# Performance work log

Hardware: AMD Instinct MI355X
Metric: run time of the kernel (lower is better)

The kernel has to match this reference:

```python
import jax, jax.numpy as jnp
import numpy as np

B, D, C, H = 16384, 512, 4096, 1024

def setup_inputs() -> dict:
    key = jax.random.key(0)
    k1, k2, k3, k4 = jax.random.split(key, 4)
    x = jax.random.normal(k1, (B, D), dtype=jnp.float32)
    centers = jax.random.normal(k2, (C, D), dtype=jnp.float32)
    # nn.Linear(C, H): weight [H, C], bias [H]
    W1 = jax.random.normal(k3, (H, C), dtype=jnp.float32) * (1.0 / np.sqrt(C))
    b1 = jax.random.normal(k4, (H,), dtype=jnp.float32) * 0.01
    return {"x": x, "centers": centers, "W1": W1, "b1": b1, "sigma": 1}


def reference(x, centers, W1, b1, sigma):
    sigma = jnp.float32(sigma)
    # Pairwise Euclidean distances via dot-product expansion (fused, no [B,C,D] tensor)
    x2 = jnp.sum(x * x, axis=-1, keepdims=True)            # [B, 1]
    c2 = jnp.sum(centers * centers, axis=-1)               # [C]
    xc = x @ centers.T                                     # [B, C]
    d2 = jnp.maximum(x2 + c2[None, :] - 2.0 * xc, 0.0)
    dists = jnp.sqrt(d2)                                   # [B, C]
    # Note: original uses exp(-dists / (2*sigma)) with UNSQUARED distance
    phi = jnp.exp(-dists / (2.0 * sigma))
    out = jax.nn.sigmoid(phi @ W1.T + b1)                  # [B, H]
    return out
```

## Files before the change

kernel.cpp:

```cpp
#include <hip/hip_runtime.h>
#include <hip/hip_bf16.h>

#define B_ROWS 16384
#define D_DIM  512
#define C_DIM  4096
#define H_DIM  1024

typedef __attribute__((ext_vector_type(8))) short  bf16x8;
typedef __attribute__((ext_vector_type(8))) unsigned short u16x8;
typedef __attribute__((ext_vector_type(4))) float  f32x4;

#define GLB __attribute__((address_space(1)))
#define LDS __attribute__((address_space(3)))

__device__ __forceinline__ unsigned short f2bf(float f) {
    unsigned int u = __float_as_uint(f);
    unsigned int r = (u + 0x7FFFu + ((u >> 16) & 1u)) >> 16;
    return (unsigned short)r;
}

__device__ __forceinline__ void async16(const void* g, void* l) {
    __builtin_amdgcn_global_load_lds((const GLB unsigned int*)g,
                                     (LDS unsigned int*)l, 16, 0, 0);
}

__device__ __forceinline__ float read_sigma(const int* p) {
    int v = *p;
    if (v >= 1 && v < (1 << 20)) return (float)v;
    return __int_as_float(v);
}

__global__ __launch_bounds__(64) void prep_rows(const float* __restrict__ in,
                                                unsigned short* __restrict__ outb,
                                                float* __restrict__ out2) {
    int row  = blockIdx.x;
    int lane = threadIdx.x;
    const float4* p = (const float4*)(in + (size_t)row * D_DIM) + lane * 2;
    float4 a = p[0], b = p[1];
    float s = a.x*a.x + a.y*a.y + a.z*a.z + a.w*a.w
            + b.x*b.x + b.y*b.y + b.z*b.z + b.w*b.w;
    u16x8 o = { f2bf(a.x), f2bf(a.y), f2bf(a.z), f2bf(a.w),
                f2bf(b.x), f2bf(b.y), f2bf(b.z), f2bf(b.w) };
    *(u16x8*)(outb + (size_t)row * D_DIM + lane * 8) = o;
#pragma unroll
    for (int off = 32; off; off >>= 1) s += __shfl_down(s, off, 64);
    if (lane == 0) out2[row] = s;
}

__global__ __launch_bounds__(256) void conv_bf16(const float* __restrict__ in,
                                                 unsigned short* __restrict__ outb,
                                                 int n8) {
    int i = blockIdx.x * 256 + threadIdx.x;
    if (i >= n8) return;
    const float4* p = (const float4*)in + (size_t)i * 2;
    float4 a = p[0], b = p[1];
    u16x8 o = { f2bf(a.x), f2bf(a.y), f2bf(a.z), f2bf(a.w),
                f2bf(b.x), f2bf(b.y), f2bf(b.z), f2bf(b.w) };
    *((u16x8*)outb + i) = o;
}

__device__ __forceinline__ void stage_tile(const unsigned short* __restrict__ g,
                                           int ld, int rowBase, int k0,
                                           unsigned short* lds, int tid) {
#pragma unroll
    for (int i = 0; i < 4; i++) {
        int idx = i * 256 + tid;
        int row = idx >> 3;
        int cc  = (idx & 7) ^ (row & 7);
        const unsigned short* src = g + (size_t)(rowBase + row) * ld + k0 + cc * 8;
        unsigned short* dst = lds + (size_t)(i * 256 + (tid & 192)) * 8;
        async16(src, dst);
    }
}

__device__ __forceinline__ void mma_k64(const unsigned short* As,
                                        const unsigned short* Bs,
                                        f32x4 (&acc)[4][4], int wr, int wc, int l) {
#pragma unroll
    for (int kk = 0; kk < 2; kk++) {
        int kc = kk * 4 + (l >> 4);
        bf16x8 a[4], b[4];
#pragma unroll
        for (int m = 0; m < 4; m++) {
            int r = wr + m * 16 + (l & 15);
            a[m] = *(const bf16x8*)(As + r * 64 + ((kc ^ (r & 7)) * 8));
        }
#pragma unroll
        for (int n = 0; n < 4; n++) {
            int r = wc + n * 16 + (l & 15);
            b[n] = *(const bf16x8*)(Bs + r * 64 + ((kc ^ (r & 7)) * 8));
        }
#pragma unroll
        for (int m = 0; m < 4; m++)
#pragma unroll
            for (int n = 0; n < 4; n++)
                acc[m][n] = __builtin_amdgcn_mfma_f32_16x16x32_bf16(a[m], b[n], acc[m][n], 0, 0, 0);
    }
}

__global__ __launch_bounds__(256) void gemm1_kernel(const unsigned short* __restrict__ xb,
                                                    const unsigned short* __restrict__ cb,
                                                    const float* __restrict__ x2,
                                                    const float* __restrict__ c2,
                                                    const int* __restrict__ sigp,
                                                    unsigned short* __restrict__ phi) {
    __shared__ unsigned short As[128 * 64];
    __shared__ unsigned short Bs[128 * 64];
    int tid = threadIdx.x;
    int rowBase = blockIdx.y * 128;
    int colBase = blockIdx.x * 128;
    int l = tid & 63, w = tid >> 6;
    int wr = (w >> 1) * 64, wc = (w & 1) * 64;

    f32x4 acc[4][4] = {};
    for (int k0 = 0; k0 < D_DIM; k0 += 64) {
        stage_tile(xb, D_DIM, rowBase, k0, As, tid);
        stage_tile(cb, D_DIM, colBase, k0, Bs, tid);
        __syncthreads();
        mma_k64(As, Bs, acc, wr, wc, l);
        __syncthreads();
    }

    float inv2s = 0.5f / read_sigma(sigp);
    int r0 = rowBase + wr + (l >> 4) * 4;
    int c0 = colBase + wc + (l & 15);
#pragma unroll
    for (int m = 0; m < 4; m++) {
#pragma unroll
        for (int j = 0; j < 4; j++) {
            int row = r0 + m * 16 + j;
            float xr = x2[row];
#pragma unroll
            for (int n = 0; n < 4; n++) {
                int col = c0 + n * 16;
                float d2 = xr + c2[col] - 2.0f * acc[m][n][j];
                d2 = fmaxf(d2, 0.0f);
                float ph = __expf(-__builtin_sqrtf(d2) * inv2s);
                phi[(size_t)row * C_DIM + col] = f2bf(ph);
            }
        }
    }
}

__global__ __launch_bounds__(256) void gemm2_kernel(const unsigned short* __restrict__ phi,
                                                    const unsigned short* __restrict__ wb,
                                                    const float* __restrict__ b1,
                                                    float* __restrict__ out) {
    __shared__ unsigned short As[128 * 64];
    __shared__ unsigned short Bs[128 * 64];
    int tid = threadIdx.x;
    int rowBase = blockIdx.y * 128;
    int colBase = blockIdx.x * 128;
    int l = tid & 63, w = tid >> 6;
    int wr = (w >> 1) * 64, wc = (w & 1) * 64;

    f32x4 acc[4][4] = {};
    for (int k0 = 0; k0 < C_DIM; k0 += 64) {
        stage_tile(phi, C_DIM, rowBase, k0, As, tid);
        stage_tile(wb, C_DIM, colBase, k0, Bs, tid);
        __syncthreads();
        mma_k64(As, Bs, acc, wr, wc, l);
        __syncthreads();
    }

    int r0 = rowBase + wr + (l >> 4) * 4;
    int c0 = colBase + wc + (l & 15);
#pragma unroll
    for (int m = 0; m < 4; m++) {
#pragma unroll
        for (int j = 0; j < 4; j++) {
            int row = r0 + m * 16 + j;
#pragma unroll
            for (int n = 0; n < 4; n++) {
                int col = c0 + n * 16;
                float z = acc[m][n][j] + b1[col];
                out[(size_t)row * H_DIM + col] = 1.0f / (1.0f + __expf(-z));
            }
        }
    }
}

extern "C" void kernel_launch(void* const* d_in, const int* in_sizes, int n_in,
                              void* d_out, int out_size, void* d_ws, size_t ws_size,
                              hipStream_t stream) {
    const float* x       = (const float*)d_in[0];
    const float* centers = (const float*)d_in[1];
    const float* W1      = (const float*)d_in[2];
    const float* b1      = (const float*)d_in[3];
    const int*   sig     = (const int*)d_in[4];
    float* out = (float*)d_out;

    char* ws = (char*)d_ws;
    unsigned short* phi = (unsigned short*)(ws);
    unsigned short* xb  = (unsigned short*)(ws + 134217728);
    unsigned short* cb  = (unsigned short*)(ws + 150994944);
    unsigned short* wb  = (unsigned short*)(ws + 155189248);
    float* x2 = (float*)(ws + 163577856);
    float* c2 = (float*)(ws + 163643392);

    prep_rows<<<B_ROWS, 64, 0, stream>>>(x, xb, x2);
    prep_rows<<<C_DIM, 64, 0, stream>>>(centers, cb, c2);
    conv_bf16<<<(H_DIM * C_DIM / 8 + 255) / 256, 256, 0, stream>>>(W1, wb, H_DIM * C_DIM / 8);

    gemm1_kernel<<<dim3(C_DIM / 128, B_ROWS / 128), 256, 0, stream>>>(xb, cb, x2, c2, sig, phi);
    gemm2_kernel<<<dim3(H_DIM / 128, B_ROWS / 128), 256, 0, stream>>>(phi, wb, b1, out);
}
```

Baseline: 415.4 us.

## Rewrite GEMMs with 256x256 tiles, double-buffered async LDS pipeline, and XCD-aware block mapping

Both GEMMs move from 128x128 tiles with 256 threads and a single LDS buffer to 256x256 tiles with 512 threads (8 waves) and double-buffered LDS. Each k-tile is split into four MFMA phases interleaved with barriers, fragment loads and async global-to-LDS prefetch of the next tile, with s_setprio raising priority during MFMA bursts. A 1D grid is remapped so consecutive blocks are spread across the 8 XCDs for L2 locality. The goal is to hide memory latency and increase data reuse per block. The cost is much higher register pressure (128 accumulator floats per lane), 128KB of LDS per block, and lower occupancy.

```diff
diff --git a/kernel.cpp b/kernel.cpp
--- a/kernel.cpp
+++ b/kernel.cpp
@@ -12,6 +12,8 @@
 
 #define GLB __attribute__((address_space(1)))
 #define LDS __attribute__((address_space(3)))
+
+#define MFMA(d, va, vb) d = __builtin_amdgcn_mfma_f32_16x16x32_bf16(va, vb, d, 0, 0, 0)
 
 __device__ __forceinline__ unsigned short f2bf(float f) {
     unsigned int u = __float_as_uint(f);
@@ -59,82 +61,159 @@
     *((u16x8*)outb + i) = o;
 }
 
-__device__ __forceinline__ void stage_tile(const unsigned short* __restrict__ g,
+__device__ __forceinline__ void stage_half(const unsigned short* __restrict__ g,
                                            int ld, int rowBase, int k0,
                                            unsigned short* lds, int tid) {
 #pragma unroll
-    for (int i = 0; i < 4; i++) {
-        int idx = i * 256 + tid;
+    for (int i = 0; i < 2; i++) {
+        int idx = i * 512 + tid;
         int row = idx >> 3;
         int cc  = (idx & 7) ^ (row & 7);
         const unsigned short* src = g + (size_t)(rowBase + row) * ld + k0 + cc * 8;
-        unsigned short* dst = lds + (size_t)(i * 256 + (tid & 192)) * 8;
+        unsigned short* dst = lds + (i * 512 + (tid & 448)) * 8;
         async16(src, dst);
     }
 }
 
-__device__ __forceinline__ void mma_k64(const unsigned short* As,
-                                        const unsigned short* Bs,
-                                        f32x4 (&acc)[4][4], int wr, int wc, int l) {
-#pragma unroll
-    for (int kk = 0; kk < 2; kk++) {
-        int kc = kk * 4 + (l >> 4);
-        bf16x8 a[4], b[4];
-#pragma unroll
-        for (int m = 0; m < 4; m++) {
-            int r = wr + m * 16 + (l & 15);
-            a[m] = *(const bf16x8*)(As + r * 64 + ((kc ^ (r & 7)) * 8));
-        }
-#pragma unroll
-        for (int n = 0; n < 4; n++) {
-            int r = wc + n * 16 + (l & 15);
-            b[n] = *(const bf16x8*)(Bs + r * 64 + ((kc ^ (r & 7)) * 8));
-        }
-#pragma unroll
-        for (int m = 0; m < 4; m++)
-#pragma unroll
-            for (int n = 0; n < 4; n++)
-                acc[m][n] = __builtin_amdgcn_mfma_f32_16x16x32_bf16(a[m], b[n], acc[m][n], 0, 0, 0);
-    }
-}
-
-__global__ __launch_bounds__(256) void gemm1_kernel(const unsigned short* __restrict__ xb,
+__device__ __forceinline__ bf16x8 frag(const unsigned short* T, int r, int kc) {
+    return *(const bf16x8*)(T + r * 64 + ((kc ^ (r & 7)) << 3));
+}
+
+__device__ __forceinline__ void ktile(unsigned short* __restrict__ Ap,
+                                      unsigned short* __restrict__ Bp,
+                                      const unsigned short* __restrict__ gA, int lda, int aRow0,
+                                      const unsigned short* __restrict__ gB, int ldb, int bRow0,
+                                      int kNext, bool doStage,
+                                      f32x4 (&acc)[8][4], int tid, int l, int AR, int BC) {
+    const int lr = l & 15, hi = l >> 4;
+    bf16x8 a[4][2], b0[2][2], b1[2][2];
+
+#pragma unroll
+    for (int m = 0; m < 4; m++) { int r = AR + m * 16 + lr;
+#pragma unroll
+        for (int kk = 0; kk < 2; kk++) a[m][kk] = frag(Ap, r, kk * 4 + hi); }
+#pragma unroll
+    for (int n = 0; n < 2; n++) { int r = BC + n * 16 + lr;
+#pragma unroll
+        for (int kk = 0; kk < 2; kk++) b0[n][kk] = frag(Bp, r, kk * 4 + hi); }
+    __builtin_amdgcn_s_barrier();
+    __builtin_amdgcn_s_setprio(1);
+#pragma unroll
+    for (int m = 0; m < 4; m++)
+#pragma unroll
+        for (int n = 0; n < 2; n++)
+#pragma unroll
+            for (int kk = 0; kk < 2; kk++) MFMA(acc[m][n], a[m][kk], b0[n][kk]);
+    __builtin_amdgcn_s_setprio(0);
+    __builtin_amdgcn_s_barrier();
+
+#pragma unroll
+    for (int n = 0; n < 2; n++) { int r = BC + (n + 2) * 16 + lr;
+#pragma unroll
+        for (int kk = 0; kk < 2; kk++) b1[n][kk] = frag(Bp, r, kk * 4 + hi); }
+    __builtin_amdgcn_s_barrier();
+    __builtin_amdgcn_s_setprio(1);
+#pragma unroll
+    for (int m = 0; m < 4; m++)
+#pragma unroll
+        for (int n = 0; n < 2; n++)
+#pragma unroll
+            for (int kk = 0; kk < 2; kk++) MFMA(acc[m][2 + n], a[m][kk], b1[n][kk]);
+    __builtin_amdgcn_s_setprio(0);
+    __builtin_amdgcn_s_barrier();
+
+#pragma unroll
+    for (int m = 0; m < 4; m++) { int r = AR + (m + 4) * 16 + lr;
+#pragma unroll
+        for (int kk = 0; kk < 2; kk++) a[m][kk] = frag(Ap, r, kk * 4 + hi); }
+    if (doStage) {
+        stage_half(gB, ldb, bRow0,       kNext, Bp,        tid);
+        stage_half(gB, ldb, bRow0 + 128, kNext, Bp + 8192, tid);
+    }
+    __builtin_amdgcn_s_barrier();
+    __builtin_amdgcn_s_setprio(1);
+#pragma unroll
+    for (int m = 0; m < 4; m++)
+#pragma unroll
+        for (int n = 0; n < 2; n++)
+#pragma unroll
+            for (int kk = 0; kk < 2; kk++) MFMA(acc[4 + m][n], a[m][kk], b0[n][kk]);
+    __builtin_amdgcn_s_setprio(0);
+    __builtin_amdgcn_s_barrier();
+
+    if (doStage) {
+        stage_half(gA, lda, aRow0,       kNext, Ap,        tid);
+        stage_half(gA, lda, aRow0 + 128, kNext, Ap + 8192, tid);
+    }
+    __builtin_amdgcn_s_barrier();
+    __builtin_amdgcn_s_setprio(1);
+#pragma unroll
+    for (int m = 0; m < 4; m++)
+#pragma unroll
+        for (int n = 0; n < 2; n++)
+#pragma unroll
+            for (int kk = 0; kk < 2; kk++) MFMA(acc[4 + m][2 + n], a[m][kk], b1[n][kk]);
+    __builtin_amdgcn_s_setprio(0);
+    asm volatile("s_waitcnt vmcnt(8)" ::: "memory");
+    __builtin_amdgcn_s_barrier();
+}
+
+__device__ __forceinline__ void gemm_core(const unsigned short* __restrict__ gA, int lda, int aRow0,
+                                          const unsigned short* __restrict__ gB, int ldb, int bRow0,
+                                          int nt, f32x4 (&acc)[8][4],
+                                          unsigned short (&As)[2][16384],
+                                          unsigned short (&Bs)[2][16384],
+                                          int tid, int l, int AR, int BC) {
+    stage_half(gA, lda, aRow0,       0,  As[0],        tid);
+    stage_half(gA, lda, aRow0 + 128, 0,  As[0] + 8192, tid);
+    stage_half(gB, ldb, bRow0,       0,  Bs[0],        tid);
+    stage_half(gB, ldb, bRow0 + 128, 0,  Bs[0] + 8192, tid);
+    stage_half(gA, lda, aRow0,       64, As[1],        tid);
+    stage_half(gA, lda, aRow0 + 128, 64, As[1] + 8192, tid);
+    stage_half(gB, ldb, bRow0,       64, Bs[1],        tid);
+    stage_half(gB, ldb, bRow0 + 128, 64, Bs[1] + 8192, tid);
+    asm volatile("s_waitcnt vmcnt(8)" ::: "memory");
+    __builtin_amdgcn_s_barrier();
+
+    for (int t = 0; t < nt; t += 2) {
+        ktile(As[0], Bs[0], gA, lda, aRow0, gB, ldb, bRow0, (t + 2) * 64, t + 2 < nt,
+              acc, tid, l, AR, BC);
+        ktile(As[1], Bs[1], gA, lda, aRow0, gB, ldb, bRow0, (t + 3) * 64, t + 3 < nt,
+              acc, tid, l, AR, BC);
+    }
+}
+
+__global__ __launch_bounds__(512) void gemm1_kernel(const unsigned short* __restrict__ xb,
                                                     const unsigned short* __restrict__ cb,
                                                     const float* __restrict__ x2,
                                                     const float* __restrict__ c2,
                                                     const int* __restrict__ sigp,
                                                     unsigned short* __restrict__ phi) {
-    __shared__ unsigned short As[128 * 64];
-    __shared__ unsigned short Bs[128 * 64];
+    __shared__ unsigned short As[2][16384];
+    __shared__ unsigned short Bs[2][16384];
     int tid = threadIdx.x;
-    int rowBase = blockIdx.y * 128;
-    int colBase = blockIdx.x * 128;
-    int l = tid & 63, w = tid >> 6;
-    int wr = (w >> 1) * 64, wc = (w & 1) * 64;
-
-    f32x4 acc[4][4] = {};
-    for (int k0 = 0; k0 < D_DIM; k0 += 64) {
-        stage_tile(xb, D_DIM, rowBase, k0, As, tid);
-        stage_tile(cb, D_DIM, colBase, k0, Bs, tid);
-        __syncthreads();
-        mma_k64(As, Bs, acc, wr, wc, l);
-        __syncthreads();
-    }
+    int nwg = gridDim.x, cpx = nwg >> 3, bid = blockIdx.x;
+    int nb = (bid & 7) * cpx + (bid >> 3);
+    const int nbx = C_DIM / 256;
+    int aRow0 = (nb / nbx) * 256, bRow0 = (nb % nbx) * 256;
+    int l = tid & 63, wid = tid >> 6;
+    int AR = (wid >> 2) * 128, BC = (wid & 3) * 64;
+
+    f32x4 acc[8][4] = {};
+    gemm_core(xb, D_DIM, aRow0, cb, D_DIM, bRow0, D_DIM / 64, acc, As, Bs, tid, l, AR, BC);
 
     float inv2s = 0.5f / read_sigma(sigp);
-    int r0 = rowBase + wr + (l >> 4) * 4;
-    int c0 = colBase + wc + (l & 15);
-#pragma unroll
-    for (int m = 0; m < 4; m++) {
+    int lr = l & 15, hi = l >> 4;
+#pragma unroll
+    for (int m = 0; m < 8; m++) {
 #pragma unroll
         for (int j = 0; j < 4; j++) {
-            int row = r0 + m * 16 + j;
+            int row = aRow0 + AR + m * 16 + hi * 4 + j;
             float xr = x2[row];
 #pragma unroll
             for (int n = 0; n < 4; n++) {
-                int col = c0 + n * 16;
-                float d2 = xr + c2[col] - 2.0f * acc[m][n][j];
-                d2 = fmaxf(d2, 0.0f);
+                int col = bRow0 + BC + n * 16 + lr;
+                float d2 = fmaxf(xr + c2[col] - 2.0f * acc[m][n][j], 0.0f);
                 float ph = __expf(-__builtin_sqrtf(d2) * inv2s);
                 phi[(size_t)row * C_DIM + col] = f2bf(ph);
             }
@@ -142,37 +221,32 @@
     }
 }
 
-__global__ __launch_bounds__(256) void gemm2_kernel(const unsigned short* __restrict__ phi,
+__global__ __launch_bounds__(512) void gemm2_kernel(const unsigned short* __restrict__ phi,
                                                     const unsigned short* __restrict__ wb,
                                                     const float* __restrict__ b1,
                                                     float* __restrict__ out) {
-    __shared__ unsigned short As[128 * 64];
-    __shared__ unsigned short Bs[128 * 64];
+    __shared__ unsigned short As[2][16384];
+    __shared__ unsigned short Bs[2][16384];
     int tid = threadIdx.x;
-    int rowBase = blockIdx.y * 128;
-    int colBase = blockIdx.x * 128;
-    int l = tid & 63, w = tid >> 6;
-    int wr = (w >> 1) * 64, wc = (w & 1) * 64;
-
-    f32x4 acc[4][4] = {};
-    for (int k0 = 0; k0 < C_DIM; k0 += 64) {
-        stage_tile(phi, C_DIM, rowBase, k0, As, tid);
-        stage_tile(wb, C_DIM, colBase, k0, Bs, tid);
-        __syncthreads();
-        mma_k64(As, Bs, acc, wr, wc, l);
-        __syncthreads();
-    }
-
-    int r0 = rowBase + wr + (l >> 4) * 4;
-    int c0 = colBase + wc + (l & 15);
-#pragma unroll
-    for (int m = 0; m < 4; m++) {
+    int nwg = gridDim.x, cpx = nwg >> 3, bid = blockIdx.x;
+    int nb = (bid & 7) * cpx + (bid >> 3);
+    const int nbx = H_DIM / 256;
+    int aRow0 = (nb / nbx) * 256, bRow0 = (nb % nbx) * 256;
+    int l = tid & 63, wid = tid >> 6;
+    int AR = (wid >> 2) * 128, BC = (wid & 3) * 64;
+
+    f32x4 acc[8][4] = {};
+    gemm_core(phi, C_DIM, aRow0, wb, C_DIM, bRow0, C_DIM / 64, acc, As, Bs, tid, l, AR, BC);
+
+    int lr = l & 15, hi = l >> 4;
+#pragma unroll
+    for (int m = 0; m < 8; m++) {
 #pragma unroll
         for (int j = 0; j < 4; j++) {
-            int row = r0 + m * 16 + j;
+            int row = aRow0 + AR + m * 16 + hi * 4 + j;
 #pragma unroll
             for (int n = 0; n < 4; n++) {
-                int col = c0 + n * 16;
+                int col = bRow0 + BC + n * 16 + lr;
                 float z = acc[m][n][j] + b1[col];
                 out[(size_t)row * H_DIM + col] = 1.0f / (1.0f + __expf(-z));
             }
@@ -202,6 +276,6 @@
     prep_rows<<<C_DIM, 64, 0, stream>>>(centers, cb, c2);
     conv_bf16<<<(H_DIM * C_DIM / 8 + 255) / 256, 256, 0, stream>>>(W1, wb, H_DIM * C_DIM / 8);
 
-    gemm1_kernel<<<dim3(C_DIM / 128, B_ROWS / 128), 256, 0, stream>>>(xb, cb, x2, c2, sig, phi);
-    gemm2_kernel<<<dim3(H_DIM / 128, B_ROWS / 128), 256, 0, stream>>>(phi, wb, b1, out);
-}
+    gemm1_kernel<<<(B_ROWS / 256) * (C_DIM / 256), 512, 0, stream>>>(xb, cb, x2, c2, sig, phi);
+    gemm2_kernel<<<(B_ROWS / 256) * (H_DIM / 256), 512, 0, stream>>>(phi, wb, b1, out);
+}
```

After: 341.2 us. -17.8%, faster.
